# Performance work log

Hardware: AMD Instinct MI355X
Metric: run time of the kernel (lower is better)

Reference implementation:

```python
import jax, jax.numpy as jnp
import numpy as np

B, S, D, H = 4, 2048, 1024, 16
DK = D // H


def setup_inputs() -> dict:
    key = jax.random.key(0)
    ks = jax.random.split(key, 9)
    x = jax.random.normal(ks[0], (B, S, D), dtype=jnp.float32)
    scale = 1.0 / np.sqrt(D)
    wq = jax.random.normal(ks[1], (D, D), dtype=jnp.float32) * scale
    wk = jax.random.normal(ks[2], (D, D), dtype=jnp.float32) * scale
    wv = jax.random.normal(ks[3], (D, D), dtype=jnp.float32) * scale
    wo = jax.random.normal(ks[4], (D, D), dtype=jnp.float32) * scale
    bq = jax.random.normal(ks[5], (D,), dtype=jnp.float32) * 0.01
    bk = jax.random.normal(ks[6], (D,), dtype=jnp.float32) * 0.01
    bv = jax.random.normal(ks[7], (D,), dtype=jnp.float32) * 0.01
    bo = jax.random.normal(ks[8], (D,), dtype=jnp.float32) * 0.01
    # causal mask: True where scores should be masked to -inf (j > i)
    mask = jnp.triu(jnp.ones((S, S), dtype=bool), k=1)[None, None, :, :]
    return {"x": x, "wq": wq, "bq": bq, "wk": wk, "bk": bk,
            "wv": wv, "bv": bv, "wo": wo, "bo": bo, "mask": mask}


def reference(x, wq, bq, wk, bk, wv, bv, wo, bo, mask):
    b, s, _ = x.shape
    # projections
    q = (x @ wq + bq).reshape(b, s, H, DK).transpose(0, 2, 1, 3)  # [B,H,S,DK]
    k = (x @ wk + bk).reshape(b, s, H, DK).transpose(0, 2, 1, 3)
    v = (x @ wv + bv).reshape(b, s, H, DK).transpose(0, 2, 1, 3)
    scores = jnp.einsum("bhqd,bhkd->bhqk", q, k) / np.sqrt(DK)
    scores = jnp.where(mask, -jnp.inf, scores)
    attn = jax.nn.softmax(scores, axis=-1)  # dropout p=0.0 -> identity
    out = jnp.einsum("bhqk,bhkd->bhqd", attn, v)
    out = out.transpose(0, 2, 1, 3).reshape(b, s, D)
    return out @ wo + bo
```

## Files before the change

### kernel.cpp

```cpp
#include <hip/hip_runtime.h>


typedef __attribute__((ext_vector_type(8))) short short8;
typedef __attribute__((ext_vector_type(4))) float floatx4;
typedef __attribute__((ext_vector_type(4))) unsigned short ushort4v;

#define SCLF (0.125f * 1.44269504f)

__device__ __forceinline__ unsigned short f2bf(float f) {
    unsigned int u = __float_as_uint(f);
    unsigned int r = (u + 0x7fffu + ((u >> 16) & 1u)) >> 16;
    return (unsigned short)r;
}

__device__ __forceinline__ unsigned int pk2bf(float lo, float hi) {
    return __builtin_amdgcn_perm(__float_as_uint(hi), __float_as_uint(lo), 0x07060302u);
}

__device__ __forceinline__ void gll16(const unsigned short* g, unsigned short* l) {
    __builtin_amdgcn_global_load_lds(
        (const __attribute__((address_space(1))) unsigned int*)g,
        (__attribute__((address_space(3))) unsigned int*)l, 16, 0, 0);
}

__device__ __forceinline__ void xcd_tile_sq(int nx, int& m0, int& n0) {
    int lid = blockIdx.y * nx + blockIdx.x;
    int grp = lid & 7;
    int inner = lid >> 3;
    int my = grp * 4 + inner / nx;
    int mx = inner % nx;
    m0 = my * 256;
    n0 = mx * 256;
}

__device__ __forceinline__ void xcd_tile_hw(int nx, int& m0, int& n0) {
    int lid = blockIdx.y * nx + blockIdx.x;
    int grp = lid & 7;
    int inner = lid >> 3;
    int my = grp * 4 + (inner & 3);
    int mx = inner >> 2;
    m0 = my * 256;
    n0 = mx * 128;
}

__global__ void cvtx_kernel(const float* __restrict__ x, unsigned short* __restrict__ xb) {
    int i = (blockIdx.x * 256 + threadIdx.x) * 4;
    float4 v = *(const float4*)&x[i];
    ushort4v o;
    o.x = f2bf(v.x); o.y = f2bf(v.y); o.z = f2bf(v.z); o.w = f2bf(v.w);
    *(ushort4v*)&xb[i] = o;
}

__global__ void wtrans_kernel(const float* __restrict__ wq, const float* __restrict__ wk,
                              const float* __restrict__ wv, const float* __restrict__ wo,
                              unsigned short* __restrict__ wtbase) {
    __shared__ float t[32][33];
    int z = blockIdx.z;
    const float* w = (z == 0) ? wq : (z == 1) ? wk : (z == 2) ? wv : wo;
    unsigned short* wt = wtbase + ((long)z << 20);
    int kb = blockIdx.y * 32, nb = blockIdx.x * 32;
    int col = threadIdx.x & 31, rw = threadIdx.x >> 5;
#pragma unroll
    for (int i = 0; i < 4; i++) {
        int row = rw + i * 8;
        t[row][col] = w[(kb + row) * 1024 + nb + col];
    }
    __syncthreads();
#pragma unroll
    for (int i = 0; i < 4; i++) {
        int row = rw + i * 8;
        wt[(nb + row) * 1024 + kb + col] = f2bf(t[col][row]);
    }
}

__device__ __forceinline__ short8 ldsr(const unsigned short* p) { return *(const short8*)p; }

#define ASQ (256 * 64)
#define BUFSQ (2 * ASQ)

template <bool SW>
__device__ __forceinline__ void gemm_core256sq(const unsigned short* __restrict__ A,
                                               const unsigned short* __restrict__ Bt,
                                               unsigned short* lds,
                                               int m0, int n0, floatx4 (&acc)[8][4]) {
    const int K = 1024, NT = 16;
    int tid = threadIdx.x;
    int lane = tid & 63, wave = tid >> 6;
    int wm = wave >> 2, wn = wave & 3;
    int quad = lane >> 4, l15 = lane & 15, l7 = l15 & 7;
    int rsub = lane >> 3;
    int gl = (lane & 7) ^ rsub;

    floatx4 zero4 = {0.f, 0.f, 0.f, 0.f};
#pragma unroll
    for (int i = 0; i < 8; i++)
#pragma unroll
        for (int j = 0; j < 4; j++) acc[i][j] = zero4;

    auto stageA = [&](int kt, int half) {
        const unsigned short* Ag = A + (long)m0 * K + kt * 64;
        unsigned short* as = lds + (kt & 1) * BUFSQ;
#pragma unroll
        for (int p = 0; p < 2; p++) {
            int chunk = half * 16 + wave * 2 + p;
            gll16(&Ag[(chunk * 8 + rsub) * K + gl * 8], &as[chunk * 512 + lane * 8]);
        }
    };
    auto stageB = [&](int kt, int half) {
        const unsigned short* Bg = Bt + (long)n0 * K + kt * 64;
        unsigned short* bs = lds + (kt & 1) * BUFSQ + ASQ;
#pragma unroll
        for (int p = 0; p < 2; p++) {
            int chunk = half * 16 + wave * 2 + p;
            gll16(&Bg[(chunk * 8 + rsub) * K + gl * 8], &bs[chunk * 512 + lane * 8]);
        }
    };

    stageA(0, 0); stageA(0, 1); stageB(0, 0); stageB(0, 1);
    stageB(1, 0); stageA(1, 0); stageB(1, 1);
    asm volatile("s_waitcnt vmcnt(6)" ::: "memory");
    __builtin_amdgcn_s_barrier();
    asm volatile("" ::: "memory");

    short8 af[4][2], b0[2][2], b1[2][2];

    for (int kt = 0; kt < NT; kt++) {
        const unsigned short* as = lds + (kt & 1) * BUFSQ;
        const unsigned short* bs = as + ASQ;

#pragma unroll
        for (int i = 0; i < 4; i++) {
            int r = wm * 128 + i * 16 + l15;
            af[i][0] = ldsr(&as[r * 64 + ((quad ^ l7) * 8)]);
            af[i][1] = ldsr(&as[r * 64 + (((4 + quad) ^ l7) * 8)]);
        }
#pragma unroll
        for (int j = 0; j < 2; j++) {
            int r = wn * 64 + j * 16 + l15;
            b0[j][0] = ldsr(&bs[r * 64 + ((quad ^ l7) * 8)]);
            b0[j][1] = ldsr(&bs[r * 64 + (((4 + quad) ^ l7) * 8)]);
        }
        if (kt + 1 < NT) stageA(kt + 1, 1);
        asm volatile("" ::: "memory");
        __builtin_amdgcn_s_barrier();
        asm volatile("s_waitcnt lgkmcnt(0)" ::: "memory");
        __builtin_amdgcn_sched_barrier(0);
        __builtin_amdgcn_s_setprio(1);
#pragma unroll
        for (int i = 0; i < 4; i++)
#pragma unroll
            for (int j = 0; j < 2; j++)
#pragma unroll
                for (int kk = 0; kk < 2; kk++)
                    acc[i][j] = SW
                        ? __builtin_amdgcn_mfma_f32_16x16x32_bf16(b0[j][kk], af[i][kk], acc[i][j], 0, 0, 0)
                        : __builtin_amdgcn_mfma_f32_16x16x32_bf16(af[i][kk], b0[j][kk], acc[i][j], 0, 0, 0);
        __builtin_amdgcn_s_setprio(0);
        asm volatile("" ::: "memory");
        __builtin_amdgcn_s_barrier();
        asm volatile("" ::: "memory");

#pragma unroll
        for (int j = 0; j < 2; j++) {
            int r = wn * 64 + (2 + j) * 16 + l15;
            b1[j][0] = ldsr(&bs[r * 64 + ((quad ^ l7) * 8)]);
            b1[j][1] = ldsr(&bs[r * 64 + (((4 + quad) ^ l7) * 8)]);
        }
        asm volatile("" ::: "memory");
        __builtin_amdgcn_s_barrier();
        asm volatile("s_waitcnt lgkmcnt(0)" ::: "memory");
        __builtin_amdgcn_sched_barrier(0);
        __builtin_amdgcn_s_setprio(1);
#pragma unroll
        for (int i = 0; i < 4; i++)
#pragma unroll
            for (int j = 0; j < 2; j++)
#pragma unroll
                for (int kk = 0; kk < 2; kk++)
                    acc[i][2 + j] = SW
                        ? __builtin_amdgcn_mfma_f32_16x16x32_bf16(b1[j][kk], af[i][kk], acc[i][2 + j], 0, 0, 0)
                        : __builtin_amdgcn_mfma_f32_16x16x32_bf16(af[i][kk], b1[j][kk], acc[i][2 + j], 0, 0, 0);
        __builtin_amdgcn_s_setprio(0);
        asm volatile("" ::: "memory");
        __builtin_amdgcn_s_barrier();
        asm volatile("" ::: "memory");

#pragma unroll
        for (int i = 0; i < 4; i++) {
            int r = wm * 128 + 64 + i * 16 + l15;
            af[i][0] = ldsr(&as[r * 64 + ((quad ^ l7) * 8)]);
            af[i][1] = ldsr(&as[r * 64 + (((4 + quad) ^ l7) * 8)]);
        }
        if (kt + 2 < NT) stageB(kt + 2, 0);
        asm volatile("" ::: "memory");
        __builtin_amdgcn_s_barrier();
        asm volatile("s_waitcnt lgkmcnt(0)" ::: "memory");
        __builtin_amdgcn_sched_barrier(0);
        __builtin_amdgcn_s_setprio(1);
#pragma unroll
        for (int i = 0; i < 4; i++)
#pragma unroll
            for (int j = 0; j < 2; j++)
#pragma unroll
                for (int kk = 0; kk < 2; kk++)
                    acc[4 + i][2 + j] = SW
                        ? __builtin_amdgcn_mfma_f32_16x16x32_bf16(b1[j][kk], af[i][kk], acc[4 + i][2 + j], 0, 0, 0)
                        : __builtin_amdgcn_mfma_f32_16x16x32_bf16(af[i][kk], b1[j][kk], acc[4 + i][2 + j], 0, 0, 0);
        __builtin_amdgcn_s_setprio(0);
        asm volatile("" ::: "memory");
        __builtin_amdgcn_s_barrier();
        asm volatile("" ::: "memory");

        if (kt + 2 < NT) { stageA(kt + 2, 0); stageB(kt + 2, 1); }
        __builtin_amdgcn_s_setprio(1);
#pragma unroll
        for (int i = 0; i < 4; i++)
#pragma unroll
            for (int j = 0; j < 2; j++)
#pragma unroll
                for (int kk = 0; kk < 2; kk++)
                    acc[4 + i][j] = SW
                        ? __builtin_amdgcn_mfma_f32_16x16x32_bf16(b0[j][kk], af[i][kk], acc[4 + i][j], 0, 0, 0)
                        : __builtin_amdgcn_mfma_f32_16x16x32_bf16(af[i][kk], b0[j][kk], acc[4 + i][j], 0, 0, 0);
        __builtin_amdgcn_s_setprio(0);
        if (kt + 2 < NT) {
            asm volatile("s_waitcnt vmcnt(6)" ::: "memory");
        } else if (kt + 1 < NT) {
            asm volatile("s_waitcnt vmcnt(0)" ::: "memory");
        }
        __builtin_amdgcn_s_barrier();
        asm volatile("" ::: "memory");
    }
}

#define A3 (256 * 64)
#define B3 (128 * 64)
#define BUF3 (A3 + B3)

template <bool SW>
__device__ __forceinline__ void gemm_core256(const unsigned short* __restrict__ A,
                                             const unsigned short* __restrict__ Bt,
                                             unsigned short* lds,
                                             int m0, int n0, floatx4 (&acc)[8][2]) {
    const int K = 1024, NT = 16;
    int tid = threadIdx.x;
    int lane = tid & 63, wave = tid >> 6;
    int wm = wave >> 2, wn = wave & 3;
    int quad = lane >> 4, l15 = lane & 15, l7 = l15 & 7;
    int rsub = lane >> 3;
    int gl = (lane & 7) ^ rsub;

    floatx4 zero4 = {0.f, 0.f, 0.f, 0.f};
#pragma unroll
    for (int i = 0; i < 8; i++)
#pragma unroll
        for (int j = 0; j < 2; j++) acc[i][j] = zero4;

    auto stage = [&](int kt, int b) {
        const unsigned short* Ag = A + (long)m0 * K + kt * 64;
        const unsigned short* Bg = Bt + (long)n0 * K + kt * 64;
        unsigned short* as = lds + b * BUF3;
        unsigned short* bs = as + A3;
#pragma unroll
        for (int p = 0; p < 4; p++) {
            int chunk = wave * 4 + p;
            gll16(&Ag[(chunk * 8 + rsub) * K + gl * 8], &as[chunk * 512 + lane * 8]);
        }
#pragma unroll
        for (int p = 0; p < 2; p++) {
            int chunk = wave * 2 + p;
            gll16(&Bg[(chunk * 8 + rsub) * K + gl * 8], &bs[chunk * 512 + lane * 8]);
        }
    };

    stage(0, 0);
    stage(1, 1);
    stage(2, 2);
    asm volatile("s_waitcnt vmcnt(12)" ::: "memory");
    __builtin_amdgcn_s_barrier();
    asm volatile("" ::: "memory");

    int buf = 0;
    for (int kt = 0; kt < NT; kt++) {
        const unsigned short* as = lds + buf * BUF3;
        const unsigned short* bs = as + A3;
        short8 bf[2][2], af[4][2], ag[4][2];
#pragma unroll
        for (int j = 0; j < 2; j++) {
            int rb = wn * 32 + j * 16 + l15;
#pragma unroll
            for (int kk = 0; kk < 2; kk++)
                bf[j][kk] = ldsr(&bs[rb * 64 + (((kk * 4 + quad) ^ l7) * 8)]);
        }
#pragma unroll
        for (int i = 0; i < 4; i++) {
            int r = wm * 128 + i * 16 + l15;
#pragma unroll
            for (int kk = 0; kk < 2; kk++)
                af[i][kk] = ldsr(&as[r * 64 + (((kk * 4 + quad) ^ l7) * 8)]);
        }
        __builtin_amdgcn_s_setprio(1);
#pragma unroll
        for (int i = 0; i < 4; i++)
#pragma unroll
            for (int j = 0; j < 2; j++)
#pragma unroll
                for (int kk = 0; kk < 2; kk++)
                    acc[i][j] = SW
                        ? __builtin_amdgcn_mfma_f32_16x16x32_bf16(bf[j][kk], af[i][kk], acc[i][j], 0, 0, 0)
                        : __builtin_amdgcn_mfma_f32_16x16x32_bf16(af[i][kk], bf[j][kk], acc[i][j], 0, 0, 0);
        __builtin_amdgcn_s_setprio(0);
#pragma unroll
        for (int i = 0; i < 4; i++) {
            int r = wm * 128 + 64 + i * 16 + l15;
#pragma unroll
            for (int kk = 0; kk < 2; kk++)
                ag[i][kk] = ldsr(&as[r * 64 + (((kk * 4 + quad) ^ l7) * 8)]);
        }
        __builtin_amdgcn_s_setprio(1);
#pragma unroll
        for (int i = 0; i < 4; i++)
#pragma unroll
            for (int j = 0; j < 2; j++)
#pragma unroll
                for (int kk = 0; kk < 2; kk++)
                    acc[4 + i][j] = SW
                        ? __builtin_amdgcn_mfma_f32_16x16x32_bf16(bf[j][kk], ag[i][kk], acc[4 + i][j], 0, 0, 0)
                        : __builtin_amdgcn_mfma_f32_16x16x32_bf16(ag[i][kk], bf[j][kk], acc[4 + i][j], 0, 0, 0);
        __builtin_amdgcn_s_setprio(0);
        asm volatile("" ::: "memory");
        __builtin_amdgcn_s_barrier();
        asm volatile("" ::: "memory");
        if (kt + 3 < NT) {
            stage(kt + 3, buf);
            asm volatile("s_waitcnt vmcnt(12)" ::: "memory");
        } else if (kt + 3 == NT) {
            asm volatile("s_waitcnt vmcnt(6)" ::: "memory");
        } else if (kt + 2 == NT) {
            asm volatile("s_waitcnt vmcnt(0)" ::: "memory");
        }
        __builtin_amdgcn_s_barrier();
        asm volatile("" ::: "memory");
        buf = (buf == 2) ? 0 : buf + 1;
    }
}

__global__ __launch_bounds__(512, 2) void projA_kernel(
    const unsigned short* __restrict__ xb, const unsigned short* __restrict__ wt,
    const float* __restrict__ bq, const float* __restrict__ bk,
    unsigned short* __restrict__ qo, unsigned short* __restrict__ ko) {
    extern __shared__ __align__(16) unsigned short smem[];
    int m0, n0;
    xcd_tile_sq(8, m0, n0);
    int tid = threadIdx.x, lane = tid & 63, wave = tid >> 6;
    int wm = wave >> 2, wn = wave & 3, quad = lane >> 4, l15 = lane & 15;
    floatx4 acc[8][4];

    gemm_core256sq<true>(xb, wt, smem, m0, n0, acc);
    int which = n0 >> 10;
    const float* bias = which ? bk : bq;
    unsigned short* dst = which ? ko : qo;
    float sc = which ? 1.0f : SCLF;
#pragma unroll
    for (int mt = 0; mt < 8; mt++)
#pragma unroll
        for (int nt = 0; nt < 4; nt++) {
            int tok = m0 + wm * 128 + mt * 16 + l15;
            int b = tok >> 11, s = tok & 2047;
            int colf = (n0 + wn * 64 + nt * 16 + quad * 4) & 1023;
            float4 bb = *(const float4*)&bias[colf];
            int h = colf >> 6, dk = colf & 63;
            ushort4v o;
            o.x = f2bf((acc[mt][nt][0] + bb.x) * sc);
            o.y = f2bf((acc[mt][nt][1] + bb.y) * sc);
            o.z = f2bf((acc[mt][nt][2] + bb.z) * sc);
            o.w = f2bf((acc[mt][nt][3] + bb.w) * sc);
            *(ushort4v*)&dst[((long)((b * 16 + h) * 2048 + s)) * 64 + dk] = o;
        }
}

__global__ __launch_bounds__(512, 2) void projB_kernel(
    const unsigned short* __restrict__ xb, const unsigned short* __restrict__ wt,
    const float* __restrict__ bv, unsigned short* __restrict__ vo) {
    extern __shared__ __align__(16) unsigned short smem[];
    int m0, n0;
    xcd_tile_hw(8, m0, n0);
    n0 += 2048;
    int tid = threadIdx.x, lane = tid & 63, wave = tid >> 6;
    int wm = wave >> 2, wn = wave & 3, quad = lane >> 4, l15 = lane & 15;
    floatx4 acc[8][2];
    gemm_core256<false>(xb, wt, smem, m0, n0, acc);
#pragma unroll
    for (int mt = 0; mt < 8; mt++)
#pragma unroll
        for (int nt = 0; nt < 2; nt++) {
            int tok0 = m0 + wm * 128 + mt * 16 + quad * 4;
            int b = tok0 >> 11, s = tok0 & 2047;
            int colf = (n0 & 1023) + wn * 32 + nt * 16 + l15;
            int h = colf >> 6, dk = colf & 63;
            float bb = bv[colf];
            ushort4v o;
            o.x = f2bf(acc[mt][nt][0] + bb);
            o.y = f2bf(acc[mt][nt][1] + bb);
            o.z = f2bf(acc[mt][nt][2] + bb);
            o.w = f2bf(acc[mt][nt][3] + bb);
            *(ushort4v*)&vo[((long)((b * 16 + h) * 64 + dk)) * 2048 + s] = o;
        }
}

__global__ __launch_bounds__(512, 2) void gemm_out_kernel(
    const unsigned short* __restrict__ ob, const unsigned short* __restrict__ wto,
    const float* __restrict__ bo, float* __restrict__ out) {
    extern __shared__ __align__(16) unsigned short smem[];
    int m0, n0;
    xcd_tile_hw(8, m0, n0);
    int tid = threadIdx.x, lane = tid & 63, wave = tid >> 6;
    int wm = wave >> 2, wn = wave & 3, quad = lane >> 4, l15 = lane & 15;
    floatx4 acc[8][2];
    gemm_core256<true>(ob, wto, smem, m0, n0, acc);

#pragma unroll
    for (int mt = 0; mt < 8; mt++)
#pragma unroll
        for (int nt = 0; nt < 2; nt++) {
            int tok = m0 + wm * 128 + mt * 16 + l15;
            int cg = n0 + wn * 32 + nt * 16 + quad * 4;
            float4 bb = *(const float4*)&bo[cg];
            float4 o;
            o.x = acc[mt][nt][0] + bb.x;
            o.y = acc[mt][nt][1] + bb.y;
            o.z = acc[mt][nt][2] + bb.z;
            o.w = acc[mt][nt][3] + bb.w;
            *(float4*)&out[(long)tok * 1024 + cg] = o;
        }
}

__device__ __forceinline__ void stage_kv(const unsigned short* __restrict__ Kg,
                                         const unsigned short* __restrict__ Vg,
                                         unsigned short* Ks, unsigned short* Vs,
                                         int lane, int wave) {
    int rsub = lane >> 3;
    int g = (lane & 7) ^ rsub;
#pragma unroll
    for (int p = 0; p < 2; p++) {
        int chunk = wave * 2 + p;
        int r = chunk * 8 + rsub;
        gll16(&Kg[r * 64 + g * 8], &Ks[chunk * 512]);
        gll16(&Vg[r * 2048 + g * 8], &Vs[chunk * 512]);
    }
}

__global__ __launch_bounds__(256, 4) void attn_kernel(
    const unsigned short* __restrict__ Q, const unsigned short* __restrict__ Kk,
    const unsigned short* __restrict__ Vt, unsigned short* __restrict__ O) {
    __shared__ __align__(16) unsigned short Ks[2][8 * 512];
    __shared__ __align__(16) unsigned short Vs[2][8 * 512];
    __shared__ __align__(16) unsigned short Ps[4 * 16 * 64];

    int bid = blockIdx.x;
    int qt = (int)((0x765489AB3210CDEFull >> ((bid >> 6) * 4)) & 15);
    int bh = bid & 63;
    int q0 = qt * 128;
    long base = (long)bh * 2048 * 64;
    long vbase = (long)bh * 64 * 2048;
    int tid = threadIdx.x, lane = tid & 63, wave = tid >> 6;
    int quad = lane >> 4, l15 = lane & 15, l7 = l15 & 7;

    short8 qfA[2], qfB[2];
    int qrA = q0 + wave * 16 + l15;
    int qrB = qrA + 64;
    qfA[0] = *(const short8*)&Q[base + qrA * 64 + quad * 8];
    qfA[1] = *(const short8*)&Q[base + qrA * 64 + 32 + quad * 8];
    qfB[0] = *(const short8*)&Q[base + qrB * 64 + quad * 8];
    qfB[1] = *(const short8*)&Q[base + qrB * 64 + 32 + quad * 8];

    float lA = 0.f, lB = 0.f;
    floatx4 oA[4], oB[4];
    floatx4 zero4 = {0.f, 0.f, 0.f, 0.f};
#pragma unroll
    for (int st = 0; st < 4; st++) { oA[st] = zero4; oB[st] = zero4; }

    unsigned short* myP = &Ps[(wave * 16) * 64];
    int pw_off = l15 * 64 + (quad & 1) * 4;
    int pr0 = l15 * 64 + ((quad ^ l7) * 8);
    int pr1 = l15 * 64 + (((4 + quad) ^ l7) * 8);

    int ktmax = 2 * qt + 1;
    stage_kv(&Kk[base], &Vt[vbase], Ks[0], Vs[0], lane, wave);
    __syncthreads();

    for (int kt = 0; kt <= ktmax; kt++) {
        int cur = kt & 1;
        if (kt < ktmax)
            stage_kv(&Kk[base + (long)(kt + 1) * 64 * 64], &Vt[vbase + (kt + 1) * 64],
                     Ks[cur ^ 1], Vs[cur ^ 1], lane, wave);
        bool doA = (kt < ktmax);
        bool maskA = (kt == ktmax - 1);
        bool maskB = (kt == ktmax);

        floatx4 saA[4], saB[4];
#pragma unroll
        for (int st = 0; st < 4; st++) {
            int row = st * 16 + l15;
            short8 kf0 = ldsr(&Ks[cur][row * 64 + ((quad ^ l7) * 8)]);
            short8 kf1 = ldsr(&Ks[cur][row * 64 + (((4 + quad) ^ l7) * 8)]);
            saB[st] = __builtin_amdgcn_mfma_f32_16x16x32_bf16(kf0, qfB[0], zero4, 0, 0, 0);
            saB[st] = __builtin_amdgcn_mfma_f32_16x16x32_bf16(kf1, qfB[1], saB[st], 0, 0, 0);
            if (doA) {
                saA[st] = __builtin_amdgcn_mfma_f32_16x16x32_bf16(kf0, qfA[0], zero4, 0, 0, 0);
                saA[st] = __builtin_amdgcn_mfma_f32_16x16x32_bf16(kf1, qfA[1], saA[st], 0, 0, 0);
            }
        }

        int kg0 = kt * 64 + quad * 4;
        short8 pfB0, pfB1, pfA0, pfA1;
        {
            float p[4][4];
#pragma unroll
            for (int st = 0; st < 4; st++)
#pragma unroll
                for (int r = 0; r < 4; r++)
                    p[st][r] = __builtin_amdgcn_exp2f(saB[st][r]);
            if (maskB) {
#pragma unroll
                for (int st = 0; st < 4; st++)
#pragma unroll
                    for (int r = 0; r < 4; r++)
                        if (kg0 + st * 16 + r > qrB) p[st][r] = 0.f;
            }
            float rs = 0.f;
#pragma unroll
            for (int st = 0; st < 4; st++) {
                rs += p[st][0] + p[st][1] + p[st][2] + p[st][3];
                uint2 pw;
                pw.x = pk2bf(p[st][0], p[st][1]);
                pw.y = pk2bf(p[st][2], p[st][3]);
                *(uint2*)&myP[pw_off + (((st * 2 + (quad >> 1)) ^ l7) * 8)] = pw;
            }
            rs += __shfl_xor(rs, 16, 64);
            rs += __shfl_xor(rs, 32, 64);
            lB += rs;
            pfB0 = ldsr(&myP[pr0]);
            pfB1 = ldsr(&myP[pr1]);
        }
        if (doA) {
            float p[4][4];
#pragma unroll
            for (int st = 0; st < 4; st++)
#pragma unroll
                for (int r = 0; r < 4; r++)
                    p[st][r] = __builtin_amdgcn_exp2f(saA[st][r]);
            if (maskA) {
#pragma unroll
                for (int st = 0; st < 4; st++)
#pragma unroll
                    for (int r = 0; r < 4; r++)
                        if (kg0 + st * 16 + r > qrA) p[st][r] = 0.f;
            }
            float rs = 0.f;
#pragma unroll
            for (int st = 0; st < 4; st++) {
                rs += p[st][0] + p[st][1] + p[st][2] + p[st][3];
                uint2 pw;
                pw.x = pk2bf(p[st][0], p[st][1]);
                pw.y = pk2bf(p[st][2], p[st][3]);
                *(uint2*)&myP[pw_off + (((st * 2 + (quad >> 1)) ^ l7) * 8)] = pw;
            }
            rs += __shfl_xor(rs, 16, 64);
            rs += __shfl_xor(rs, 32, 64);
            lA += rs;
            pfA0 = ldsr(&myP[pr0]);
            pfA1 = ldsr(&myP[pr1]);
        }

#pragma unroll
        for (int st = 0; st < 4; st++) {
            int row = st * 16 + l15;
            short8 vf0 = ldsr(&Vs[cur][row * 64 + ((quad ^ l7) * 8)]);
            short8 vf1 = ldsr(&Vs[cur][row * 64 + (((4 + quad) ^ l7) * 8)]);
            oB[st] = __builtin_amdgcn_mfma_f32_16x16x32_bf16(vf0, pfB0, oB[st], 0, 0, 0);
            oB[st] = __builtin_amdgcn_mfma_f32_16x16x32_bf16(vf1, pfB1, oB[st], 0, 0, 0);
            if (doA) {
                oA[st] = __builtin_amdgcn_mfma_f32_16x16x32_bf16(vf0, pfA0, oA[st], 0, 0, 0);
                oA[st] = __builtin_amdgcn_mfma_f32_16x16x32_bf16(vf1, pfA1, oA[st], 0, 0, 0);
            }
        }
        __syncthreads();
    }

    int b = bh >> 4, h = bh & 15;
    float invA = 1.f / lA, invB = 1.f / lB;
#pragma unroll
    for (int st = 0; st < 4; st++) {
        uint2 ov;
        ov.x = pk2bf(oA[st][0] * invA, oA[st][1] * invA);
        ov.y = pk2bf(oA[st][2] * invA, oA[st][3] * invA);
        *(uint2*)&O[((long)(b * 2048 + qrA)) * 1024 + h * 64 + st * 16 + quad * 4] = ov;
        uint2 ow;
        ow.x = pk2bf(oB[st][0] * invB, oB[st][1] * invB);
        ow.y = pk2bf(oB[st][2] * invB, oB[st][3] * invB);
        *(uint2*)&O[((long)(b * 2048 + qrB)) * 1024 + h * 64 + st * 16 + quad * 4] = ow;
    }
}

extern "C" void kernel_launch(void* const* d_in, const int* in_sizes, int n_in,
                              void* d_out, int out_size, void* d_ws, size_t ws_size,
                              hipStream_t stream) {
    const float* x  = (const float*)d_in[0];
    const float* wq = (const float*)d_in[1];
    const float* bq = (const float*)d_in[2];
    const float* wk = (const float*)d_in[3];
    const float* bk = (const float*)d_in[4];
    const float* wv = (const float*)d_in[5];
    const float* bv = (const float*)d_in[6];
    const float* wo = (const float*)d_in[7];
    const float* bo = (const float*)d_in[8];

    char* w = (char*)d_ws;
    unsigned short* xb  = (unsigned short*)w;
    unsigned short* wtq = (unsigned short*)(w + (16u << 20));
    unsigned short* wto = wtq + (3u << 20);
    unsigned short* qb  = wto + (1u << 20);
    unsigned short* kb  = qb + (8u << 20);
    unsigned short* vb  = kb + (8u << 20);
    unsigned short* ob  = vb + (8u << 20);

    cvtx_kernel<<<8192, 256, 0, stream>>>(x, xb);
    wtrans_kernel<<<dim3(32, 32, 4), 256, 0, stream>>>(wq, wk, wv, wo, wtq);
    projA_kernel<<<dim3(8, 32), 512, 128 * 1024, stream>>>(xb, wtq, bq, bk, qb, kb);
    projB_kernel<<<dim3(8, 32), 512, 144 * 1024, stream>>>(xb, wtq, bv, vb);
    attn_kernel<<<1024, 256, 0, stream>>>(qb, kb, vb, ob);
    gemm_out_kernel<<<dim3(8, 32), 512, 144 * 1024, stream>>>(ob, wto, bo, (float*)d_out);
}
```

Before: 253.1 us.

## Split KV tiles across two wave groups per attention block and merge

The attention kernel grows to 512 threads as two groups of four waves. Each group takes alternating 64-key tiles with its own double-buffered K/V staging in dynamic LDS, so each block runs half as many serial loop steps. At the end the partial outputs and row sums from one group are passed through LDS and added into the other group's before normalisation. The causal mask check now runs on every tile instead of only the diagonal ones, and A-rows are computed even on fully masked tiles. The block-to-query-tile order permutation is also changed, and the 80KB LDS per block may limit how many blocks fit on a CU.

```diff
diff --git a/kernel.cpp b/kernel.cpp
--- a/kernel.cpp
+++ b/kernel.cpp
@@ -438,36 +438,39 @@
 __device__ __forceinline__ void stage_kv(const unsigned short* __restrict__ Kg,
                                          const unsigned short* __restrict__ Vg,
                                          unsigned short* Ks, unsigned short* Vs,
-                                         int lane, int wave) {
+                                         int lane, int w4) {
     int rsub = lane >> 3;
     int g = (lane & 7) ^ rsub;
 #pragma unroll
     for (int p = 0; p < 2; p++) {
-        int chunk = wave * 2 + p;
+        int chunk = w4 * 2 + p;
         int r = chunk * 8 + rsub;
         gll16(&Kg[r * 64 + g * 8], &Ks[chunk * 512]);
         gll16(&Vg[r * 2048 + g * 8], &Vs[chunk * 512]);
     }
 }
 
-__global__ __launch_bounds__(256, 4) void attn_kernel(
+__global__ __launch_bounds__(512, 4) void attn_kernel(
     const unsigned short* __restrict__ Q, const unsigned short* __restrict__ Kk,
     const unsigned short* __restrict__ Vt, unsigned short* __restrict__ O) {
-    __shared__ __align__(16) unsigned short Ks[2][8 * 512];
-    __shared__ __align__(16) unsigned short Vs[2][8 * 512];
-    __shared__ __align__(16) unsigned short Ps[4 * 16 * 64];
+    extern __shared__ __align__(16) unsigned short smem[];
 
     int bid = blockIdx.x;
-    int qt = (int)((0x765489AB3210CDEFull >> ((bid >> 6) * 4)) & 15);
+    int qt = (int)((0x541098DC6723ABEFull >> ((bid >> 6) * 4)) & 15);
     int bh = bid & 63;
     int q0 = qt * 128;
     long base = (long)bh * 2048 * 64;
     long vbase = (long)bh * 64 * 2048;
     int tid = threadIdx.x, lane = tid & 63, wave = tid >> 6;
+    int grp = wave >> 2, w4 = wave & 3;
     int quad = lane >> 4, l15 = lane & 15, l7 = l15 & 7;
 
+    unsigned short* Kg0 = smem + grp * 2 * 4096;
+    unsigned short* Vg0 = smem + 16384 + grp * 2 * 4096;
+    unsigned short* myP = smem + 32768 + wave * 1024;
+
     short8 qfA[2], qfB[2];
-    int qrA = q0 + wave * 16 + l15;
+    int qrA = q0 + w4 * 16 + l15;
     int qrB = qrA + 64;
     qfA[0] = *(const short8*)&Q[base + qrA * 64 + quad * 8];
     qfA[1] = *(const short8*)&Q[base + qrA * 64 + 32 + quad * 8];
@@ -480,54 +483,47 @@
 #pragma unroll
     for (int st = 0; st < 4; st++) { oA[st] = zero4; oB[st] = zero4; }
 
-    unsigned short* myP = &Ps[(wave * 16) * 64];
     int pw_off = l15 * 64 + (quad & 1) * 4;
     int pr0 = l15 * 64 + ((quad ^ l7) * 8);
     int pr1 = l15 * 64 + (((4 + quad) ^ l7) * 8);
 
-    int ktmax = 2 * qt + 1;
-    stage_kv(&Kk[base], &Vt[vbase], Ks[0], Vs[0], lane, wave);
+    int niter = qt + 1;
+    stage_kv(&Kk[base + (long)grp * 64 * 64], &Vt[vbase + grp * 64],
+             Kg0, Vg0, lane, w4);
     __syncthreads();
 
-    for (int kt = 0; kt <= ktmax; kt++) {
-        int cur = kt & 1;
-        if (kt < ktmax)
-            stage_kv(&Kk[base + (long)(kt + 1) * 64 * 64], &Vt[vbase + (kt + 1) * 64],
-                     Ks[cur ^ 1], Vs[cur ^ 1], lane, wave);
-        bool doA = (kt < ktmax);
-        bool maskA = (kt == ktmax - 1);
-        bool maskB = (kt == ktmax);
+    for (int i = 0; i < niter; i++) {
+        int t = 2 * i + grp;
+        int cur = i & 1;
+        unsigned short* Ks = Kg0 + cur * 4096;
+        unsigned short* Vs = Vg0 + cur * 4096;
+        if (i + 1 < niter)
+            stage_kv(&Kk[base + (long)(t + 2) * 64 * 64], &Vt[vbase + (t + 2) * 64],
+                     Kg0 + (cur ^ 1) * 4096, Vg0 + (cur ^ 1) * 4096, lane, w4);
 
         floatx4 saA[4], saB[4];
 #pragma unroll
         for (int st = 0; st < 4; st++) {
             int row = st * 16 + l15;
-            short8 kf0 = ldsr(&Ks[cur][row * 64 + ((quad ^ l7) * 8)]);
-            short8 kf1 = ldsr(&Ks[cur][row * 64 + (((4 + quad) ^ l7) * 8)]);
+            short8 kf0 = ldsr(&Ks[row * 64 + ((quad ^ l7) * 8)]);
+            short8 kf1 = ldsr(&Ks[row * 64 + (((4 + quad) ^ l7) * 8)]);
             saB[st] = __builtin_amdgcn_mfma_f32_16x16x32_bf16(kf0, qfB[0], zero4, 0, 0, 0);
             saB[st] = __builtin_amdgcn_mfma_f32_16x16x32_bf16(kf1, qfB[1], saB[st], 0, 0, 0);
-            if (doA) {
-                saA[st] = __builtin_amdgcn_mfma_f32_16x16x32_bf16(kf0, qfA[0], zero4, 0, 0, 0);
-                saA[st] = __builtin_amdgcn_mfma_f32_16x16x32_bf16(kf1, qfA[1], saA[st], 0, 0, 0);
-            }
-        }
-
-        int kg0 = kt * 64 + quad * 4;
+            saA[st] = __builtin_amdgcn_mfma_f32_16x16x32_bf16(kf0, qfA[0], zero4, 0, 0, 0);
+            saA[st] = __builtin_amdgcn_mfma_f32_16x16x32_bf16(kf1, qfA[1], saA[st], 0, 0, 0);
+        }
+
+        int kg0 = t * 64 + quad * 4;
         short8 pfB0, pfB1, pfA0, pfA1;
         {
             float p[4][4];
 #pragma unroll
             for (int st = 0; st < 4; st++)
 #pragma unroll
-                for (int r = 0; r < 4; r++)
+                for (int r = 0; r < 4; r++) {
                     p[st][r] = __builtin_amdgcn_exp2f(saB[st][r]);
-            if (maskB) {
-#pragma unroll
-                for (int st = 0; st < 4; st++)
-#pragma unroll
-                    for (int r = 0; r < 4; r++)
-                        if (kg0 + st * 16 + r > qrB) p[st][r] = 0.f;
-            }
+                    if (kg0 + st * 16 + r > qrB) p[st][r] = 0.f;
+                }
             float rs = 0.f;
 #pragma unroll
             for (int st = 0; st < 4; st++) {
@@ -543,20 +539,15 @@
             pfB0 = ldsr(&myP[pr0]);
             pfB1 = ldsr(&myP[pr1]);
         }
-        if (doA) {
+        {
             float p[4][4];
 #pragma unroll
             for (int st = 0; st < 4; st++)
 #pragma unroll
-                for (int r = 0; r < 4; r++)
+                for (int r = 0; r < 4; r++) {
                     p[st][r] = __builtin_amdgcn_exp2f(saA[st][r]);
-            if (maskA) {
-#pragma unroll
-                for (int st = 0; st < 4; st++)
-#pragma unroll
-                    for (int r = 0; r < 4; r++)
-                        if (kg0 + st * 16 + r > qrA) p[st][r] = 0.f;
-            }
+                    if (kg0 + st * 16 + r > qrA) p[st][r] = 0.f;
+                }
             float rs = 0.f;
 #pragma unroll
             for (int st = 0; st < 4; st++) {
@@ -576,30 +567,53 @@
 #pragma unroll
         for (int st = 0; st < 4; st++) {
             int row = st * 16 + l15;
-            short8 vf0 = ldsr(&Vs[cur][row * 64 + ((quad ^ l7) * 8)]);
-            short8 vf1 = ldsr(&Vs[cur][row * 64 + (((4 + quad) ^ l7) * 8)]);
+            short8 vf0 = ldsr(&Vs[row * 64 + ((quad ^ l7) * 8)]);
+            short8 vf1 = ldsr(&Vs[row * 64 + (((4 + quad) ^ l7) * 8)]);
             oB[st] = __builtin_amdgcn_mfma_f32_16x16x32_bf16(vf0, pfB0, oB[st], 0, 0, 0);
             oB[st] = __builtin_amdgcn_mfma_f32_16x16x32_bf16(vf1, pfB1, oB[st], 0, 0, 0);
-            if (doA) {
-                oA[st] = __builtin_amdgcn_mfma_f32_16x16x32_bf16(vf0, pfA0, oA[st], 0, 0, 0);
-                oA[st] = __builtin_amdgcn_mfma_f32_16x16x32_bf16(vf1, pfA1, oA[st], 0, 0, 0);
+            oA[st] = __builtin_amdgcn_mfma_f32_16x16x32_bf16(vf0, pfA0, oA[st], 0, 0, 0);
+            oA[st] = __builtin_amdgcn_mfma_f32_16x16x32_bf16(vf1, pfA1, oA[st], 0, 0, 0);
+        }
+        __syncthreads();
+    }
+
+    float* xch = (float*)smem;
+    int slot = w4 * 64 + lane;
+    if (grp == 1) {
+#pragma unroll
+        for (int st = 0; st < 4; st++)
+#pragma unroll
+            for (int r = 0; r < 4; r++) {
+                xch[(st * 4 + r) * 256 + slot] = oA[st][r];
+                xch[(16 + st * 4 + r) * 256 + slot] = oB[st][r];
             }
-        }
-        __syncthreads();
-    }
-
-    int b = bh >> 4, h = bh & 15;
-    float invA = 1.f / lA, invB = 1.f / lB;
-#pragma unroll
-    for (int st = 0; st < 4; st++) {
-        uint2 ov;
-        ov.x = pk2bf(oA[st][0] * invA, oA[st][1] * invA);
-        ov.y = pk2bf(oA[st][2] * invA, oA[st][3] * invA);
-        *(uint2*)&O[((long)(b * 2048 + qrA)) * 1024 + h * 64 + st * 16 + quad * 4] = ov;
-        uint2 ow;
-        ow.x = pk2bf(oB[st][0] * invB, oB[st][1] * invB);
-        ow.y = pk2bf(oB[st][2] * invB, oB[st][3] * invB);
-        *(uint2*)&O[((long)(b * 2048 + qrB)) * 1024 + h * 64 + st * 16 + quad * 4] = ow;
+        xch[32 * 256 + slot] = lA;
+        xch[33 * 256 + slot] = lB;
+    }
+    __syncthreads();
+    if (grp == 0) {
+        float invA = 1.f / (lA + xch[32 * 256 + slot]);
+        float invB = 1.f / (lB + xch[33 * 256 + slot]);
+        int b = bh >> 4, h = bh & 15;
+#pragma unroll
+        for (int st = 0; st < 4; st++) {
+            float a0 = oA[st][0] + xch[(st * 4 + 0) * 256 + slot];
+            float a1 = oA[st][1] + xch[(st * 4 + 1) * 256 + slot];
+            float a2 = oA[st][2] + xch[(st * 4 + 2) * 256 + slot];
+            float a3 = oA[st][3] + xch[(st * 4 + 3) * 256 + slot];
+            uint2 ov;
+            ov.x = pk2bf(a0 * invA, a1 * invA);
+            ov.y = pk2bf(a2 * invA, a3 * invA);
+            *(uint2*)&O[((long)(b * 2048 + qrA)) * 1024 + h * 64 + st * 16 + quad * 4] = ov;
+            float b0_ = oB[st][0] + xch[(16 + st * 4 + 0) * 256 + slot];
+            float b1_ = oB[st][1] + xch[(16 + st * 4 + 1) * 256 + slot];
+            float b2_ = oB[st][2] + xch[(16 + st * 4 + 2) * 256 + slot];
+            float b3_ = oB[st][3] + xch[(16 + st * 4 + 3) * 256 + slot];
+            uint2 ow;
+            ow.x = pk2bf(b0_ * invB, b1_ * invB);
+            ow.y = pk2bf(b2_ * invB, b3_ * invB);
+            *(uint2*)&O[((long)(b * 2048 + qrB)) * 1024 + h * 64 + st * 16 + quad * 4] = ow;
+        }
     }
 }
 
@@ -629,6 +643,6 @@
     wtrans_kernel<<<dim3(32, 32, 4), 256, 0, stream>>>(wq, wk, wv, wo, wtq);
     projA_kernel<<<dim3(8, 32), 512, 128 * 1024, stream>>>(xb, wtq, bq, bk, qb, kb);
     projB_kernel<<<dim3(8, 32), 512, 144 * 1024, stream>>>(xb, wtq, bv, vb);
-    attn_kernel<<<1024, 256, 0, stream>>>(qb, kb, vb, ob);
+    attn_kernel<<<1024, 512, 80 * 1024, stream>>>(qb, kb, vb, ob);
     gemm_out_kernel<<<dim3(8, 32), 512, 144 * 1024, stream>>>(ob, wto, bo, (float*)d_out);
 }
```

Result: slower. 283.2 us (+11.9%).
